# Performance work log

Hardware: AMD Instinct MI355X
Metric: run time of the kernel (lower is better)

The kernel has to match this reference:

```python
import jax, jax.numpy as jnp
import numpy as np

EPS = 1e-5
KH = KW = 3
PAD = 1

def conv3x3(x, w, b=None):
    out = jax.lax.conv_general_dilated(
        x, w, window_strides=(1, 1), padding=((PAD, PAD), (PAD, PAD)),
        dimension_numbers=("NCHW", "OIHW", "NCHW"))
    if b is not None:
        out = out + b[None, :, None, None]
    return out

def batchnorm(x, gamma, beta):
    # training-mode BatchNorm2d: batch statistics over (N, H, W)
    mean = x.mean(axis=(0, 2, 3), keepdims=True)
    var = x.var(axis=(0, 2, 3), keepdims=True)
    return gamma[None, :, None, None] * (x - mean) / jnp.sqrt(var + EPS) + beta[None, :, None, None]

def bilinear_gather(x, y_pos, x_pos):
    # x: [B,C,H,W]; y_pos/x_pos: [B,P,H,W] (P = KH*KW sampling taps)
    # zero padding outside image (mmcv modulated deform conv semantics)
    B, C, H, W = x.shape
    P = y_pos.shape[1]
    x_flat = x.reshape(B, C, H * W)
    y0 = jnp.floor(y_pos)
    x0 = jnp.floor(x_pos)
    ly = y_pos - y0
    lx = x_pos - x0
    out = jnp.zeros((B, C, P, H, W), dtype=x.dtype)
    for dy, dx, wgt in ((0, 0, (1 - ly) * (1 - lx)), (0, 1, (1 - ly) * lx),
                        (1, 0, ly * (1 - lx)), (1, 1, ly * lx)):
        yi = y0 + dy
        xi = x0 + dx
        valid = ((yi >= 0) & (yi <= H - 1) & (xi >= 0) & (xi <= W - 1)).astype(x.dtype)
        yc = jnp.clip(yi, 0, H - 1).astype(jnp.int32)
        xc = jnp.clip(xi, 0, W - 1).astype(jnp.int32)
        idx = (yc * W + xc).reshape(B, 1, P * H * W)
        vals = jnp.take_along_axis(x_flat, jnp.broadcast_to(idx, (B, C, P * H * W)), axis=2)
        vals = vals.reshape(B, C, P, H, W)
        out = out + vals * (wgt * valid)[:, None]
    return out  # [B,C,P,H,W]

def modulated_deform_conv(x, w_off, b_off, w_dcn):
    B, C, H, W = x.shape
    P = KH * KW
    off = conv3x3(x, w_off, b_off)  # [B, 3*P, H, W]
    o1, o2, m = jnp.split(off, 3, axis=1)
    offset = jnp.concatenate([o1, o2], axis=1)            # [B, 2P, H, W]
    offset = offset.reshape(B, P, 2, H, W)                # channel 2p -> dy, 2p+1 -> dx
    mask = jax.nn.sigmoid(m)                              # [B, P, H, W]
    hh = jnp.arange(H, dtype=x.dtype)
    ww = jnp.arange(W, dtype=x.dtype)
    ky = jnp.arange(KH, dtype=x.dtype)
    kx = jnp.arange(KW, dtype=x.dtype)
    # base sampling grid per tap p = ky*KW + kx: (h - PAD + ky, w - PAD + kx)
    base_y = (hh[None, :] - PAD + ky[:, None])            # [KH, H]
    base_x = (ww[None, :] - PAD + kx[:, None])            # [KW, W]
    base_y = jnp.broadcast_to(base_y[:, None, :, None], (KH, KW, H, W)).reshape(P, H, W)
    base_x = jnp.broadcast_to(base_x[None, :, None, :], (KH, KW, H, W)).reshape(P, H, W)
    y_pos = base_y[None] + offset[:, :, 0]                # [B,P,H,W]
    x_pos = base_x[None] + offset[:, :, 1]
    sampled = bilinear_gather(x, y_pos, x_pos)            # [B,C,P,H,W]
    sampled = sampled * mask[:, None]
    w = w_dcn.reshape(w_dcn.shape[0], C, P)               # [O, C, P]
    return jnp.einsum("bcphw,ocp->bohw", sampled, w)

def setup_inputs() -> dict:
    key = jax.random.key(0)
    ks = jax.random.split(key, 10)
    B, Ch, H, W = 4, 256, 64, 64
    Cin, Cout = 2 * Ch, 256
    P = KH * KW
    inp = {
        "input_v": jax.random.normal(ks[0], (B, Ch, H, W), jnp.float32),
        "input_i": jax.random.normal(ks[1], (B, Ch, H, W), jnp.float32),
        "w_off": jax.random.normal(ks[2], (3 * P, Cin, KH, KW), jnp.float32) * 0.01,
        "b_off": jnp.zeros((3 * P,), jnp.float32),
        "w_dcn": jax.random.normal(ks[3], (Cout, Cin, KH, KW), jnp.float32) * (1.0 / np.sqrt(Cin * P)),
        "gamma1": jnp.ones((Cout,), jnp.float32),
        "beta1": jnp.zeros((Cout,), jnp.float32),
        "w2": jax.random.normal(ks[4], (Cout, Cout, KH, KW), jnp.float32) * (1.0 / np.sqrt(Cout * P)),
        "gamma2": jnp.ones((Cout,), jnp.float32),
        "beta2": jnp.zeros((Cout,), jnp.float32),
    }
    return inp

def reference(input_v, input_i, w_off, b_off, w_dcn, gamma1, beta1, w2, gamma2, beta2):
    x = jnp.concatenate([input_v, input_i], axis=1)
    out = modulated_deform_conv(x, w_off, b_off, w_dcn)
    out = jax.nn.relu(batchnorm(out, gamma1, beta1))
    out = jax.nn.relu(batchnorm(conv3x3(out, w2), gamma2, beta2))
    return out
```

## Files before the change

### kernel.cpp

```cpp
#include <hip/hip_runtime.h>
#include <cstdint>
#include <cstddef>

typedef unsigned short u16;
typedef __attribute__((ext_vector_type(8))) short s16x8;
typedef __attribute__((ext_vector_type(4))) float f32x4;

#define DEV __device__ __forceinline__

DEV float bf2f(short u){
  union { unsigned int i; float f; } v;
  v.i = ((unsigned int)(u16)u) << 16;
  return v.f;
}
DEV short f2bf(float f){
  union { float f; unsigned int i; } v; v.f = f;
  unsigned int u = v.i;
  u += 0x7fffu + ((u >> 16) & 1u);
  return (short)(u >> 16);
}
DEV f32x4 f32x4_zero(){
  f32x4 z;
#pragma unroll
  for(int j=0;j<4;j++) z[j]=0.f;
  return z;
}
DEV f32x4 mfma16(s16x8 a, s16x8 b, f32x4 c){
  return __builtin_amdgcn_mfma_f32_16x16x32_bf16(a, b, c, 0, 0, 0);
}
DEV void cp16(const void* g, void* l){
  __builtin_amdgcn_global_load_lds(
      (const __attribute__((address_space(1))) unsigned int*)g,
      (__attribute__((address_space(3))) unsigned int*)l, 16, 0, 0);
}

static constexpr size_t OFF_ACC_B   = 0;
static constexpr size_t OUT1_ACC_B  = 2097152;
static constexpr size_t OUT2_ACC_B  = 18874368;
static constexpr size_t STATS_B     = 35651584;
static constexpr size_t ZERO_BYTES  = 35655680;
static constexpr size_t XN_PAD_B    = 35655680;
static constexpr size_t OUT1N_PAD_B = 53497856;
static constexpr size_t WOFFT_B     = 62418944;
static constexpr size_t WDCNT_B     = 62713856;
static constexpr size_t W2T_B       = 65073152;
static constexpr size_t SAMP_O_B    = 66252800;
static constexpr size_t SAMP_W_B    = 68612096;
static constexpr size_t A_SAMP_B    = 70971392;

__global__ void k_border(u16* __restrict__ xp, u16* __restrict__ op){
  const int cid = blockIdx.x, t = threadIdx.x;
  const int b = cid / 260, rem = cid % 260;
  int y, x;
  if(rem < 132){ y = (rem/66)*65; x = rem%66; }
  else { int r2 = rem-132; x = (r2>>6)*65; y = 1 + (r2&63); }
  const size_t cell = (size_t)(b*66+y)*66 + x;
  ((unsigned int*)(xp + cell*512))[t] = 0;
  if(t < 128) ((unsigned int*)(op + cell*256))[t] = 0;
}

__global__ void k_x_to_nhwc(const float* __restrict__ v, const float* __restrict__ vi,
                            u16* __restrict__ xn){
  __shared__ float tile[64][65];
  const int b = blockIdx.z, c0 = blockIdx.y*64, h = blockIdx.x;
  const float* src = (c0 < 256) ? (v  + ((size_t)b*256 + c0)      *4096)
                                : (vi + ((size_t)b*256 + (c0-256))*4096);
  const int t = threadIdx.x;
#pragma unroll
  for(int k=0;k<16;k++){
    int idx = t + k*256;
    int cl = idx >> 6, wl = idx & 63;
    tile[cl][wl] = src[(size_t)cl*4096 + h*64 + wl];
  }
  __syncthreads();
#pragma unroll
  for(int k=0;k<16;k++){
    int idx = t + k*256;
    int wl = idx >> 6, cl = idx & 63;
    xn[((size_t)(b*66 + h+1)*66 + (wl+1))*512 + c0 + cl] = (u16)f2bf(tile[cl][wl]);
  }
}

__global__ void k_prep_woff(const float* __restrict__ w, u16* __restrict__ wt){
  int i = blockIdx.x*256 + threadIdx.x;
  if(i >= 147456) return;
  int j = i & 7, n = (i>>3) & 31, kcp = i>>8;
  int kc = kcp & 63, tp = kcp >> 6;
  int c = kc*8 + j;
  float val = (n < 27) ? w[(size_t)(n*512 + c)*9 + tp] : 0.f;
  wt[i] = (u16)f2bf(val);
}
__global__ void k_prep_wdcn(const float* __restrict__ w, u16* __restrict__ wt){
  int i = blockIdx.x*256 + threadIdx.x;
  if(i >= 1179648) return;
  int j = i & 7, n = (i>>3) & 255, kcp = i>>11;
  int kc = kcp & 63, tp = kcp >> 6;
  int c = kc*8 + j;
  wt[i] = (u16)f2bf(w[(size_t)(n*512 + c)*9 + tp]);
}
__global__ void k_prep_w2(const float* __restrict__ w, u16* __restrict__ wt){
  int i = blockIdx.x*256 + threadIdx.x;
  if(i >= 589824) return;
  int j = i & 7, n = (i>>3) & 255, kcp = i>>11;
  int kc = kcp & 31, tp = kcp >> 5;
  int c = kc*8 + j;
  wt[i] = (u16)f2bf(w[(size_t)(n*256 + c)*9 + tp]);
}

__global__ __launch_bounds__(256, 6) void k_conv_off(
    const u16* __restrict__ xn, const u16* __restrict__ wt, float* __restrict__ offa){
  __shared__ short A[2][4][64][8];
  __shared__ short B[2][4][32][8];
  const int tid = threadIdx.x;
  const int lane = tid & 63, wid = tid >> 6;
  const int quad = lane >> 4, ln = lane & 15;
  const int m0 = blockIdx.x * 64;
  const int b = m0 >> 12, h = (m0 >> 6) & 63;
  const int gst0 = blockIdx.y * 24;
  const int m_base = wid * 16;
  f32x4 acc0 = f32x4_zero(), acc1 = f32x4_zero();

  {
    const int tp = gst0 >> 4, s = gst0 & 15;
    const int ty = tp/3, tx = tp - ty*3;
    cp16(xn + ((size_t)(b*66 + h+ty)*66 + lane + tx)*512 + s*32 + wid*8, &A[0][wid][0][0]);
    if(wid < 2)
      cp16(wt + ((size_t)tp*64 + s*4)*256 + wid*512 + lane*8, (short*)&B[0][0][0][0] + wid*512);
  }
  __syncthreads();

  int buf = 0;
  for(int it=0; it<24; it++){
    const int nb = buf ^ 1;
    if(it < 23){
      const int gn = gst0 + it + 1;
      const int tp = gn >> 4, s = gn & 15;
      const int ty = tp/3, tx = tp - ty*3;
      cp16(xn + ((size_t)(b*66 + h+ty)*66 + lane + tx)*512 + s*32 + wid*8, &A[nb][wid][0][0]);
      if(wid < 2)
        cp16(wt + ((size_t)tp*64 + s*4)*256 + wid*512 + lane*8, (short*)&B[nb][0][0][0] + wid*512);
    }
    const s16x8* Ap = (const s16x8*)&A[buf][0][0][0];
    const s16x8* Bp = (const s16x8*)&B[buf][0][0][0];
    s16x8 a  = Ap[quad*64 + m_base + ln];
    s16x8 b0 = Bp[quad*32 + ln];
    s16x8 b1 = Bp[quad*32 + 16 + ln];
    acc0 = mfma16(a, b0, acc0);
    acc1 = mfma16(a, b1, acc1);
    __syncthreads();
    buf = nb;
  }
#pragma unroll
  for(int nf=0;nf<2;nf++){
    const f32x4 v = nf ? acc1 : acc0;
    const int col = nf*16 + ln;
#pragma unroll
    for(int i=0;i<4;i++){
      const int row = m_base + quad*4 + i;
      unsafeAtomicAdd(offa + (size_t)(m0+row)*32 + col, v[i]);
    }
  }
}

__global__ void k_sampler(const float* __restrict__ offa, const float* __restrict__ boff,
                          int* __restrict__ so, float* __restrict__ sw){
  const int idx = blockIdx.x*256 + threadIdx.x;
  if(idx >= 16384*9) return;
  const int m = idx / 9, tp = idx - m*9;
  const int b = m >> 12, h = (m >> 6) & 63, w = m & 63;
  const float* orow = offa + (size_t)m*32;
  float dy = orow[2*tp]   + boff[2*tp];
  float dx = orow[2*tp+1] + boff[2*tp+1];
  float mz = orow[18+tp]  + boff[18+tp];
  float mk = 1.f / (1.f + expf(-mz));
  float ypos = (float)(h - 1 + tp/3) + dy;
  float xpos = (float)(w - 1 + tp%3) + dx;
  float y0f = floorf(ypos), x0f = floorf(xpos);
  float ly = ypos - y0f, lx = xpos - x0f;
  int y0 = (int)y0f, x0 = (int)x0f;
#pragma unroll
  for(int k=0;k<4;k++){
    int ddy = k >> 1, ddx = k & 1;
    int yi = y0 + ddy, xi = x0 + ddx;
    bool vv = (yi >= 0) & (yi < 64) & (xi >= 0) & (xi < 64);
    float wk = (ddy ? ly : 1.f-ly) * (ddx ? lx : 1.f-lx) * mk;
    if(!vv) wk = 0.f;
    int yc = yi < 0 ? 0 : (yi > 63 ? 63 : yi);
    int xc = xi < 0 ? 0 : (xi > 63 ? 63 : xi);
    so[(size_t)idx*4 + k] = ((b*66 + yc+1)*66 + xc+1) << 9;
    sw[(size_t)idx*4 + k] = wk;
  }
}

__global__ __launch_bounds__(256) void k_sample_a(
    const u16* __restrict__ xn, const int* __restrict__ so, const float* __restrict__ sw,
    u16* __restrict__ as){
  const int blk = blockIdx.x;
  const int pb = ((blk & 7) << 5) | (blk >> 3);
  const int m = pb*64 + (threadIdx.x >> 2);
  const int q = threadIdx.x & 3;
  for(int tp=0; tp<9; tp++){
    const int4   po = *(const int4*)  (so + ((size_t)m*9 + tp)*4);
    const float4 pw = *(const float4*)(sw + ((size_t)m*9 + tp)*4);
    const u16* x0 = xn + po.x + q*8;
    const u16* x1 = xn + po.y + q*8;
    const u16* x2 = xn + po.z + q*8;
    const u16* x3 = xn + po.w + q*8;
    u16* dst = as + (size_t)m*4608 + tp*512 + q*8;
#pragma unroll 4
    for(int u=0; u<16; u++){
      const int c0 = u*32;
      s16x8 g0 = *(const s16x8*)(x0 + c0);
      s16x8 g1 = *(const s16x8*)(x1 + c0);
      s16x8 g2 = *(const s16x8*)(x2 + c0);
      s16x8 g3 = *(const s16x8*)(x3 + c0);
      s16x8 pk;
#pragma unroll
      for(int j=0;j<8;j++){
        float f = pw.x * bf2f(g0[j]);
        f = fmaf(pw.y, bf2f(g1[j]), f);
        f = fmaf(pw.z, bf2f(g2[j]), f);
        f = fmaf(pw.w, bf2f(g3[j]), f);
        pk[j] = f2bf(f);
      }
      *(s16x8*)(dst + c0) = pk;
    }
  }
}

__global__ __launch_bounds__(256, 4) void k_dcn_gemm(
    const u16* __restrict__ as, const u16* __restrict__ wt, float* __restrict__ outa){
  __shared__ short A[2][4][64][8];
  __shared__ short B[2][4][256][8];
  const int tid = threadIdx.x;
  const int lane = tid & 63, wid = tid >> 6;
  const int quad = lane >> 4, ln = lane & 15;
  const int m0 = blockIdx.x * 64;
  const int gst0 = blockIdx.y * 48;
  const int m_base = (wid >> 1)*32, n_base = (wid & 1)*128;
  f32x4 acc[2][8];
#pragma unroll
  for(int mf=0;mf<2;mf++)
#pragma unroll
    for(int nf=0;nf<8;nf++) acc[mf][nf] = f32x4_zero();

  const u16* arow = as + (size_t)(m0 + lane)*4608;

  {
    const int tp = gst0 >> 4, s = gst0 & 15;
    cp16(arow + gst0*32 + wid*8, &A[0][wid][0][0]);
    const u16* bs = wt + ((size_t)tp*64 + s*4)*2048 + (wid*4)*512 + lane*8;
    short* bd = (short*)&B[0][0][0][0] + (wid*4)*512;
#pragma unroll
    for(int i=0;i<4;i++) cp16(bs + i*512, bd + i*512);
  }
  __syncthreads();

  int buf = 0;
  for(int it=0; it<48; it++){
    const int nb = buf ^ 1;
    if(it < 47){
      const int gn = gst0 + it + 1;
      const int tp = gn >> 4, s = gn & 15;
      cp16(arow + gn*32 + wid*8, &A[nb][wid][0][0]);
      const u16* bs = wt + ((size_t)tp*64 + s*4)*2048 + (wid*4)*512 + lane*8;
      short* bd = (short*)&B[nb][0][0][0] + (wid*4)*512;
#pragma unroll
      for(int i=0;i<4;i++) cp16(bs + i*512, bd + i*512);
    }
    const s16x8* Ap = (const s16x8*)&A[buf][0][0][0];
    const s16x8* Bp = (const s16x8*)&B[buf][0][0][0];
    s16x8 a0 = Ap[quad*64 + m_base + ln];
    s16x8 a1 = Ap[quad*64 + m_base + 16 + ln];
#pragma unroll
    for(int nf=0;nf<8;nf++){
      s16x8 bf = Bp[quad*256 + n_base + nf*16 + ln];
      acc[0][nf] = mfma16(a0, bf, acc[0][nf]);
      acc[1][nf] = mfma16(a1, bf, acc[1][nf]);
    }
    __syncthreads();
    buf = nb;
  }
#pragma unroll
  for(int mf=0;mf<2;mf++)
#pragma unroll
    for(int nf=0;nf<8;nf++){
      const int col = n_base + nf*16 + ln;
#pragma unroll
      for(int i=0;i<4;i++){
        const int row = m_base + mf*16 + quad*4 + i;
        unsafeAtomicAdd(outa + (size_t)(m0+row)*256 + col, acc[mf][nf][i]);
      }
    }
}

__global__ __launch_bounds__(256, 4) void k_conv2(
    const u16* __restrict__ a_in, const u16* __restrict__ wt, float* __restrict__ outa){
  __shared__ short A[2][4][64][8];
  __shared__ short B[2][4][256][8];
  const int tid = threadIdx.x;
  const int lane = tid & 63, wid = tid >> 6;
  const int quad = lane >> 4, ln = lane & 15;
  const int m0 = blockIdx.x * 64;
  const int b = m0 >> 12, h = (m0 >> 6) & 63;
  const int gst0 = blockIdx.y * 24;
  const int m_base = (wid >> 1)*32, n_base = (wid & 1)*128;
  f32x4 acc[2][8];
#pragma unroll
  for(int mf=0;mf<2;mf++)
#pragma unroll
    for(int nf=0;nf<8;nf++) acc[mf][nf] = f32x4_zero();

  {
    const int tp = gst0 >> 3, s = gst0 & 7;
    const int ty = tp/3, tx = tp - ty*3;
    cp16(a_in + ((size_t)(b*66 + h+ty)*66 + lane + tx)*256 + s*32 + wid*8, &A[0][wid][0][0]);
    const u16* bs = wt + ((size_t)tp*32 + s*4)*2048 + (wid*4)*512 + lane*8;
    short* bd = (short*)&B[0][0][0][0] + (wid*4)*512;
#pragma unroll
    for(int i=0;i<4;i++) cp16(bs + i*512, bd + i*512);
  }
  __syncthreads();

  int buf = 0;
  for(int it=0; it<24; it++){
    const int nb = buf ^ 1;
    if(it < 23){
      const int gn = gst0 + it + 1;
      const int tp = gn >> 3, s = gn & 7;
      const int ty = tp/3, tx = tp - ty*3;
      cp16(a_in + ((size_t)(b*66 + h+ty)*66 + lane + tx)*256 + s*32 + wid*8, &A[nb][wid][0][0]);
      const u16* bs = wt + ((size_t)tp*32 + s*4)*2048 + (wid*4)*512 + lane*8;
      short* bd = (short*)&B[nb][0][0][0] + (wid*4)*512;
#pragma unroll
      for(int i=0;i<4;i++) cp16(bs + i*512, bd + i*512);
    }
    const s16x8* Ap = (const s16x8*)&A[buf][0][0][0];
    const s16x8* Bp = (const s16x8*)&B[buf][0][0][0];
    s16x8 a0 = Ap[quad*64 + m_base + ln];
    s16x8 a1 = Ap[quad*64 + m_base + 16 + ln];
#pragma unroll
    for(int nf=0;nf<8;nf++){
      s16x8 bf = Bp[quad*256 + n_base + nf*16 + ln];
      acc[0][nf] = mfma16(a0, bf, acc[0][nf]);
      acc[1][nf] = mfma16(a1, bf, acc[1][nf]);
    }
    __syncthreads();
    buf = nb;
  }
#pragma unroll
  for(int mf=0;mf<2;mf++)
#pragma unroll
    for(int nf=0;nf<8;nf++){
      const int col = n_base + nf*16 + ln;
#pragma unroll
      for(int i=0;i<4;i++){
        const int row = m_base + mf*16 + quad*4 + i;
        unsafeAtomicAdd(outa + (size_t)(m0+row)*256 + col, acc[mf][nf][i]);
      }
    }
}

__global__ void k_stats(const float* __restrict__ acc, float* __restrict__ sum,
                        float* __restrict__ sq){
  const int m0 = blockIdx.x*64;
  const int c = threadIdx.x;
  float s = 0.f, q = 0.f;
  for(int i=0;i<64;i++){
    float v = acc[(size_t)(m0+i)*256 + c];
    s += v; q += v*v;
  }
  unsafeAtomicAdd(sum + c, s);
  unsafeAtomicAdd(sq + c, q);
}

__global__ void k_bn1(const float* __restrict__ acc, const float* __restrict__ sum,
                      const float* __restrict__ sq, const float* __restrict__ g,
                      const float* __restrict__ bt, u16* __restrict__ o){
  __shared__ float sc[256], sh[256];
  const int t = threadIdx.x;
  {
    float mean = sum[t] * (1.f/16384.f);
    float var  = sq[t] * (1.f/16384.f) - mean*mean;
    float rstd = rsqrtf(var + 1e-5f);
    float s = g[t] * rstd;
    sc[t] = s; sh[t] = bt[t] - mean*s;
  }
  __syncthreads();
  const int c4 = (t & 63) * 4;
  const float s0 = sc[c4], s1 = sc[c4+1], s2 = sc[c4+2], s3 = sc[c4+3];
  const float h0 = sh[c4], h1 = sh[c4+1], h2 = sh[c4+2], h3 = sh[c4+3];
#pragma unroll
  for(int k=0;k<4;k++){
    int m = blockIdx.x*16 + k*4 + (t>>6);
    int b = m >> 12, hh = (m >> 6) & 63, ww = m & 63;
    const float4 v = *(const float4*)(acc + (size_t)m*256 + c4);
    unsigned int lo = (unsigned int)(u16)f2bf(fmaxf(0.f, v.x*s0 + h0))
                    | ((unsigned int)(u16)f2bf(fmaxf(0.f, v.y*s1 + h1)) << 16);
    unsigned int hi = (unsigned int)(u16)f2bf(fmaxf(0.f, v.z*s2 + h2))
                    | ((unsigned int)(u16)f2bf(fmaxf(0.f, v.w*s3 + h3)) << 16);
    uint2 pr; pr.x = lo; pr.y = hi;
    *(uint2*)(o + ((size_t)(b*66 + hh+1)*66 + ww+1)*256 + c4) = pr;
  }
}

__global__ void k_bn2_out(const float* __restrict__ acc, const float* __restrict__ sum,
                          const float* __restrict__ sq, const float* __restrict__ g,
                          const float* __restrict__ bt, float* __restrict__ out){
  __shared__ float tile[64][65];
  __shared__ float sc[64], sh[64];
  const int t = threadIdx.x;
  const int b = blockIdx.z, c0 = blockIdx.y*64, hw0 = blockIdx.x*64;
  if(t < 64){
    int c = c0 + t;
    float mean = sum[c] * (1.f/16384.f);
    float var  = sq[c] * (1.f/16384.f) - mean*mean;
    float rstd = rsqrtf(var + 1e-5f);
    float s = g[c] * rstd;
    sc[t] = s; sh[t] = bt[c] - mean*s;
  }
  __syncthreads();
#pragma unroll
  for(int k=0;k<16;k++){
    int idx = t + k*256;
    int wl = idx >> 6, cl = idx & 63;
    float v = acc[(size_t)((b<<12) + hw0 + wl)*256 + c0 + cl];
    tile[wl][cl] = fmaxf(0.f, v*sc[cl] + sh[cl]);
  }
  __syncthreads();
#pragma unroll
  for(int k=0;k<16;k++){
    int idx = t + k*256;
    int cl = idx >> 6, wl = idx & 63;
    out[(size_t)(b*256 + c0 + cl)*4096 + hw0 + wl] = tile[wl][cl];
  }
}

extern "C" void kernel_launch(void* const* d_in, const int* in_sizes, int n_in,
                              void* d_out, int out_size, void* d_ws, size_t ws_size,
                              hipStream_t stream){
  const float* in_v  = (const float*)d_in[0];
  const float* in_i  = (const float*)d_in[1];
  const float* w_off = (const float*)d_in[2];
  const float* b_off = (const float*)d_in[3];
  const float* w_dcn = (const float*)d_in[4];
  const float* g1    = (const float*)d_in[5];
  const float* bt1   = (const float*)d_in[6];
  const float* w2    = (const float*)d_in[7];
  const float* g2    = (const float*)d_in[8];
  const float* bt2   = (const float*)d_in[9];
  float* out = (float*)d_out;
  char* ws = (char*)d_ws;

  float* off_acc  = (float*)(ws + OFF_ACC_B);
  float* out1_acc = (float*)(ws + OUT1_ACC_B);
  float* out2_acc = (float*)(ws + OUT2_ACC_B);
  float* stats    = (float*)(ws + STATS_B);
  float* sum1 = stats,       *sq1 = stats + 256;
  float* sum2 = stats + 512, *sq2 = stats + 768;
  u16* xn_pad    = (u16*)(ws + XN_PAD_B);
  u16* out1n_pad = (u16*)(ws + OUT1N_PAD_B);
  u16* wofft = (u16*)(ws + WOFFT_B);
  u16* wdcnt = (u16*)(ws + WDCNT_B);
  u16* w2t   = (u16*)(ws + W2T_B);
  int*   samp_o = (int*)(ws + SAMP_O_B);
  float* samp_w = (float*)(ws + SAMP_W_B);
  u16* a_samp = (u16*)(ws + A_SAMP_B);

  hipMemsetAsync(ws, 0, ZERO_BYTES, stream);
  k_border<<<1040, 256, 0, stream>>>(xn_pad, out1n_pad);
  k_x_to_nhwc<<<dim3(64,8,4), 256, 0, stream>>>(in_v, in_i, xn_pad);
  k_prep_woff<<<576, 256, 0, stream>>>(w_off, wofft);
  k_prep_wdcn<<<4608, 256, 0, stream>>>(w_dcn, wdcnt);
  k_prep_w2<<<2304, 256, 0, stream>>>(w2, w2t);
  k_conv_off<<<dim3(256,6), 256, 0, stream>>>(xn_pad, wofft, off_acc);
  k_sampler<<<576, 256, 0, stream>>>(off_acc, b_off, samp_o, samp_w);
  k_sample_a<<<256, 256, 0, stream>>>(xn_pad, samp_o, samp_w, a_samp);
  k_dcn_gemm<<<dim3(256,3), 256, 0, stream>>>(a_samp, wdcnt, out1_acc);
  k_stats<<<256, 256, 0, stream>>>(out1_acc, sum1, sq1);
  k_bn1<<<1024, 256, 0, stream>>>(out1_acc, sum1, sq1, g1, bt1, out1n_pad);
  k_conv2<<<dim3(256,3), 256, 0, stream>>>(out1n_pad, w2t, out2_acc);
  k_stats<<<256, 256, 0, stream>>>(out2_acc, sum2, sq2);
  k_bn2_out<<<dim3(64,4,4), 256, 0, stream>>>(out2_acc, sum2, sq2, g2, bt2, out);
}
```

Measured before the change: 393.1 us.

## Retile DCN and conv2 GEMMs to 128x128 and split sampling per tap

Both implicit-GEMM kernels move from a 64x256 output tile with a 32-wide K step and double-buffered LDS to a 128x128 tile with a 64-wide K step. Each wave now computes a 4x4 grid of MFMA fragments, and the grid gains a split-K z dimension. LDS staging becomes single-buffered with two barriers per iteration, so loads no longer overlap compute. The launch bound drops to 3 blocks per CU. Separately, the sampling kernel assigns one tap per block instead of looping over all 9, giving 9x more blocks to raise parallelism for the gather.

Result: faster. 382.0 us (-2.8%).

```diff
diff --git a/kernel.cpp b/kernel.cpp
--- a/kernel.cpp
+++ b/kernel.cpp
@@ -196,167 +196,166 @@
     const u16* __restrict__ xn, const int* __restrict__ so, const float* __restrict__ sw,
     u16* __restrict__ as){
   const int blk = blockIdx.x;
-  const int pb = ((blk & 7) << 5) | (blk >> 3);
+  const int x = blk & 7, g = blk >> 3;
+  const int tp = g >> 5, pbi = g & 31;
+  const int pb = x*32 + pbi;
   const int m = pb*64 + (threadIdx.x >> 2);
   const int q = threadIdx.x & 3;
-  for(int tp=0; tp<9; tp++){
-    const int4   po = *(const int4*)  (so + ((size_t)m*9 + tp)*4);
-    const float4 pw = *(const float4*)(sw + ((size_t)m*9 + tp)*4);
-    const u16* x0 = xn + po.x + q*8;
-    const u16* x1 = xn + po.y + q*8;
-    const u16* x2 = xn + po.z + q*8;
-    const u16* x3 = xn + po.w + q*8;
-    u16* dst = as + (size_t)m*4608 + tp*512 + q*8;
+  const int4   po = *(const int4*)  (so + ((size_t)m*9 + tp)*4);
+  const float4 pw = *(const float4*)(sw + ((size_t)m*9 + tp)*4);
+  const u16* x0 = xn + po.x + q*8;
+  const u16* x1 = xn + po.y + q*8;
+  const u16* x2 = xn + po.z + q*8;
+  const u16* x3 = xn + po.w + q*8;
+  u16* dst = as + (size_t)m*4608 + tp*512 + q*8;
 #pragma unroll 4
-    for(int u=0; u<16; u++){
-      const int c0 = u*32;
-      s16x8 g0 = *(const s16x8*)(x0 + c0);
-      s16x8 g1 = *(const s16x8*)(x1 + c0);
-      s16x8 g2 = *(const s16x8*)(x2 + c0);
-      s16x8 g3 = *(const s16x8*)(x3 + c0);
-      s16x8 pk;
-#pragma unroll
-      for(int j=0;j<8;j++){
-        float f = pw.x * bf2f(g0[j]);
-        f = fmaf(pw.y, bf2f(g1[j]), f);
-        f = fmaf(pw.z, bf2f(g2[j]), f);
-        f = fmaf(pw.w, bf2f(g3[j]), f);
-        pk[j] = f2bf(f);
-      }
-      *(s16x8*)(dst + c0) = pk;
-    }
-  }
-}
-
-__global__ __launch_bounds__(256, 4) void k_dcn_gemm(
+  for(int u=0; u<16; u++){
+    const int c0 = u*32;
+    s16x8 g0 = *(const s16x8*)(x0 + c0);
+    s16x8 g1 = *(const s16x8*)(x1 + c0);
+    s16x8 g2 = *(const s16x8*)(x2 + c0);
+    s16x8 g3 = *(const s16x8*)(x3 + c0);
+    s16x8 pk;
+#pragma unroll
+    for(int j=0;j<8;j++){
+      float f = pw.x * bf2f(g0[j]);
+      f = fmaf(pw.y, bf2f(g1[j]), f);
+      f = fmaf(pw.z, bf2f(g2[j]), f);
+      f = fmaf(pw.w, bf2f(g3[j]), f);
+      pk[j] = f2bf(f);
+    }
+    *(s16x8*)(dst + c0) = pk;
+  }
+}
+
+__global__ __launch_bounds__(256, 3) void k_dcn_gemm(
     const u16* __restrict__ as, const u16* __restrict__ wt, float* __restrict__ outa){
-  __shared__ short A[2][4][64][8];
-  __shared__ short B[2][4][256][8];
+  __shared__ short A[8][128][8];
+  __shared__ short B[8][128][8];
   const int tid = threadIdx.x;
   const int lane = tid & 63, wid = tid >> 6;
   const int quad = lane >> 4, ln = lane & 15;
-  const int m0 = blockIdx.x * 64;
-  const int gst0 = blockIdx.y * 48;
-  const int m_base = (wid >> 1)*32, n_base = (wid & 1)*128;
-  f32x4 acc[2][8];
-#pragma unroll
-  for(int mf=0;mf<2;mf++)
-#pragma unroll
-    for(int nf=0;nf<8;nf++) acc[mf][nf] = f32x4_zero();
-
-  const u16* arow = as + (size_t)(m0 + lane)*4608;
-
-  {
-    const int tp = gst0 >> 4, s = gst0 & 15;
-    cp16(arow + gst0*32 + wid*8, &A[0][wid][0][0]);
-    const u16* bs = wt + ((size_t)tp*64 + s*4)*2048 + (wid*4)*512 + lane*8;
-    short* bd = (short*)&B[0][0][0][0] + (wid*4)*512;
-#pragma unroll
-    for(int i=0;i<4;i++) cp16(bs + i*512, bd + i*512);
-  }
-  __syncthreads();
-
-  int buf = 0;
-  for(int it=0; it<48; it++){
-    const int nb = buf ^ 1;
-    if(it < 47){
-      const int gn = gst0 + it + 1;
-      const int tp = gn >> 4, s = gn & 15;
-      cp16(arow + gn*32 + wid*8, &A[nb][wid][0][0]);
-      const u16* bs = wt + ((size_t)tp*64 + s*4)*2048 + (wid*4)*512 + lane*8;
-      short* bd = (short*)&B[nb][0][0][0] + (wid*4)*512;
-#pragma unroll
-      for(int i=0;i<4;i++) cp16(bs + i*512, bd + i*512);
-    }
-    const s16x8* Ap = (const s16x8*)&A[buf][0][0][0];
-    const s16x8* Bp = (const s16x8*)&B[buf][0][0][0];
-    s16x8 a0 = Ap[quad*64 + m_base + ln];
-    s16x8 a1 = Ap[quad*64 + m_base + 16 + ln];
-#pragma unroll
-    for(int nf=0;nf<8;nf++){
-      s16x8 bf = Bp[quad*256 + n_base + nf*16 + ln];
-      acc[0][nf] = mfma16(a0, bf, acc[0][nf]);
-      acc[1][nf] = mfma16(a1, bf, acc[1][nf]);
+  const int m0 = blockIdx.x * 128, n0 = blockIdx.y * 128;
+  const int it0 = blockIdx.z * 24;
+  const int m_w = (wid >> 1)*64, n_w = (wid & 1)*64;
+  const s16x8* Ap = (const s16x8*)A;
+  const s16x8* Bp = (const s16x8*)B;
+  f32x4 acc[4][4];
+#pragma unroll
+  for(int mf=0;mf<4;mf++)
+#pragma unroll
+    for(int nf=0;nf<4;nf++) acc[mf][nf] = f32x4_zero();
+
+  const u16* arow0 = as + (size_t)(m0 + lane)*4608;
+  const u16* arow1 = as + (size_t)(m0 + 64 + lane)*4608;
+
+  for(int it=0; it<24; it++){
+    const int k0 = (it0 + it)*64;
+#pragma unroll
+    for(int i=0;i<4;i++){
+      const int tt = wid*4 + i, kc = tt >> 1, rh = tt & 1;
+      cp16((rh ? arow1 : arow0) + k0 + kc*8, &A[kc][rh*64][0]);
+    }
+#pragma unroll
+    for(int i=0;i<4;i++){
+      const int tt = wid*4 + i, kc = tt >> 1, nh = tt & 1;
+      cp16(wt + ((size_t)((k0>>3) + kc)*256 + n0 + nh*64 + lane)*8, &B[kc][nh*64][0]);
     }
     __syncthreads();
-    buf = nb;
-  }
-#pragma unroll
-  for(int mf=0;mf<2;mf++)
-#pragma unroll
-    for(int nf=0;nf<8;nf++){
-      const int col = n_base + nf*16 + ln;
+#pragma unroll
+    for(int ks=0; ks<2; ks++){
+      s16x8 af[4], bf[4];
+#pragma unroll
+      for(int mf=0;mf<4;mf++) af[mf] = Ap[(ks*4+quad)*128 + m_w + mf*16 + ln];
+#pragma unroll
+      for(int nf=0;nf<4;nf++) bf[nf] = Bp[(ks*4+quad)*128 + n_w + nf*16 + ln];
+#pragma unroll
+      for(int mf=0;mf<4;mf++)
+#pragma unroll
+        for(int nf=0;nf<4;nf++)
+          acc[mf][nf] = mfma16(af[mf], bf[nf], acc[mf][nf]);
+    }
+    __syncthreads();
+  }
+#pragma unroll
+  for(int mf=0;mf<4;mf++)
+#pragma unroll
+    for(int nf=0;nf<4;nf++){
+      const int col = n0 + n_w + nf*16 + ln;
 #pragma unroll
       for(int i=0;i<4;i++){
-        const int row = m_base + mf*16 + quad*4 + i;
-        unsafeAtomicAdd(outa + (size_t)(m0+row)*256 + col, acc[mf][nf][i]);
+        const int row = m0 + m_w + mf*16 + quad*4 + i;
+        unsafeAtomicAdd(outa + (size_t)row*256 + col, acc[mf][nf][i]);
       }
     }
 }
 
-__global__ __launch_bounds__(256, 4) void k_conv2(
+__global__ __launch_bounds__(256, 3) void k_conv2(
     const u16* __restrict__ a_in, const u16* __restrict__ wt, float* __restrict__ outa){
-  __shared__ short A[2][4][64][8];
-  __shared__ short B[2][4][256][8];
+  __shared__ short A[8][128][8];
+  __shared__ short B[8][128][8];
   const int tid = threadIdx.x;
   const int lane = tid & 63, wid = tid >> 6;
   const int quad = lane >> 4, ln = lane & 15;
-  const int m0 = blockIdx.x * 64;
-  const int b = m0 >> 12, h = (m0 >> 6) & 63;
-  const int gst0 = blockIdx.y * 24;
-  const int m_base = (wid >> 1)*32, n_base = (wid & 1)*128;
-  f32x4 acc[2][8];
-#pragma unroll
-  for(int mf=0;mf<2;mf++)
-#pragma unroll
-    for(int nf=0;nf<8;nf++) acc[mf][nf] = f32x4_zero();
-
-  {
-    const int tp = gst0 >> 3, s = gst0 & 7;
+  const int m0 = blockIdx.x * 128, n0 = blockIdx.y * 128;
+  const int it0 = blockIdx.z * 12;
+  const int m_w = (wid >> 1)*64, n_w = (wid & 1)*64;
+  const s16x8* Ap = (const s16x8*)A;
+  const s16x8* Bp = (const s16x8*)B;
+  f32x4 acc[4][4];
+#pragma unroll
+  for(int mf=0;mf<4;mf++)
+#pragma unroll
+    for(int nf=0;nf<4;nf++) acc[mf][nf] = f32x4_zero();
+
+  int cell[2];
+#pragma unroll
+  for(int rh=0; rh<2; rh++){
+    const int m = m0 + rh*64 + lane;
+    const int b = m >> 12, h = (m >> 6) & 63, w = m & 63;
+    cell[rh] = (b*66 + h)*66 + w;
+  }
+
+  for(int it=0; it<12; it++){
+    const int k0 = (it0 + it)*64;
+    const int tp = k0 >> 8;
     const int ty = tp/3, tx = tp - ty*3;
-    cp16(a_in + ((size_t)(b*66 + h+ty)*66 + lane + tx)*256 + s*32 + wid*8, &A[0][wid][0][0]);
-    const u16* bs = wt + ((size_t)tp*32 + s*4)*2048 + (wid*4)*512 + lane*8;
-    short* bd = (short*)&B[0][0][0][0] + (wid*4)*512;
-#pragma unroll
-    for(int i=0;i<4;i++) cp16(bs + i*512, bd + i*512);
-  }
-  __syncthreads();
-
-  int buf = 0;
-  for(int it=0; it<24; it++){
-    const int nb = buf ^ 1;
-    if(it < 23){
-      const int gn = gst0 + it + 1;
-      const int tp = gn >> 3, s = gn & 7;
-      const int ty = tp/3, tx = tp - ty*3;
-      cp16(a_in + ((size_t)(b*66 + h+ty)*66 + lane + tx)*256 + s*32 + wid*8, &A[nb][wid][0][0]);
-      const u16* bs = wt + ((size_t)tp*32 + s*4)*2048 + (wid*4)*512 + lane*8;
-      short* bd = (short*)&B[nb][0][0][0] + (wid*4)*512;
-#pragma unroll
-      for(int i=0;i<4;i++) cp16(bs + i*512, bd + i*512);
-    }
-    const s16x8* Ap = (const s16x8*)&A[buf][0][0][0];
-    const s16x8* Bp = (const s16x8*)&B[buf][0][0][0];
-    s16x8 a0 = Ap[quad*64 + m_base + ln];
-    s16x8 a1 = Ap[quad*64 + m_base + 16 + ln];
-#pragma unroll
-    for(int nf=0;nf<8;nf++){
-      s16x8 bf = Bp[quad*256 + n_base + nf*16 + ln];
-      acc[0][nf] = mfma16(a0, bf, acc[0][nf]);
-      acc[1][nf] = mfma16(a1, bf, acc[1][nf]);
+    const int kb8 = (k0 & 255) >> 3;
+#pragma unroll
+    for(int i=0;i<4;i++){
+      const int tt = wid*4 + i, kc = tt >> 1, rh = tt & 1;
+      cp16(a_in + ((size_t)(cell[rh] + ty*66 + tx))*256 + (kb8 + kc)*8, &A[kc][rh*64][0]);
+    }
+#pragma unroll
+    for(int i=0;i<4;i++){
+      const int tt = wid*4 + i, kc = tt >> 1, nh = tt & 1;
+      cp16(wt + ((size_t)((k0>>3) + kc)*256 + n0 + nh*64 + lane)*8, &B[kc][nh*64][0]);
     }
     __syncthreads();
-    buf = nb;
-  }
-#pragma unroll
-  for(int mf=0;mf<2;mf++)
-#pragma unroll
-    for(int nf=0;nf<8;nf++){
-      const int col = n_base + nf*16 + ln;
+#pragma unroll
+    for(int ks=0; ks<2; ks++){
+      s16x8 af[4], bf[4];
+#pragma unroll
+      for(int mf=0;mf<4;mf++) af[mf] = Ap[(ks*4+quad)*128 + m_w + mf*16 + ln];
+#pragma unroll
+      for(int nf=0;nf<4;nf++) bf[nf] = Bp[(ks*4+quad)*128 + n_w + nf*16 + ln];
+#pragma unroll
+      for(int mf=0;mf<4;mf++)
+#pragma unroll
+        for(int nf=0;nf<4;nf++)
+          acc[mf][nf] = mfma16(af[mf], bf[nf], acc[mf][nf]);
+    }
+    __syncthreads();
+  }
+#pragma unroll
+  for(int mf=0;mf<4;mf++)
+#pragma unroll
+    for(int nf=0;nf<4;nf++){
+      const int col = n0 + n_w + nf*16 + ln;
 #pragma unroll
       for(int i=0;i<4;i++){
-        const int row = m_base + mf*16 + quad*4 + i;
-        unsafeAtomicAdd(outa + (size_t)(m0+row)*256 + col, acc[mf][nf][i]);
+        const int row = m0 + m_w + mf*16 + quad*4 + i;
+        unsafeAtomicAdd(outa + (size_t)row*256 + col, acc[mf][nf][i]);
       }
     }
 }
@@ -475,11 +474,11 @@
   k_prep_w2<<<2304, 256, 0, stream>>>(w2, w2t);
   k_conv_off<<<dim3(256,6), 256, 0, stream>>>(xn_pad, wofft, off_acc);
   k_sampler<<<576, 256, 0, stream>>>(off_acc, b_off, samp_o, samp_w);
-  k_sample_a<<<256, 256, 0, stream>>>(xn_pad, samp_o, samp_w, a_samp);
-  k_dcn_gemm<<<dim3(256,3), 256, 0, stream>>>(a_samp, wdcnt, out1_acc);
+  k_sample_a<<<2304, 256, 0, stream>>>(xn_pad, samp_o, samp_w, a_samp);
+  k_dcn_gemm<<<dim3(128,2,3), 256, 0, stream>>>(a_samp, wdcnt, out1_acc);
   k_stats<<<256, 256, 0, stream>>>(out1_acc, sum1, sq1);
   k_bn1<<<1024, 256, 0, stream>>>(out1_acc, sum1, sq1, g1, bt1, out1n_pad);
-  k_conv2<<<dim3(256,3), 256, 0, stream>>>(out1n_pad, w2t, out2_acc);
+  k_conv2<<<dim3(128,2,3), 256, 0, stream>>>(out1n_pad, w2t, out2_acc);
   k_stats<<<256, 256, 0, stream>>>(out2_acc, sum2, sq2);
   k_bn2_out<<<dim3(64,4,4), 256, 0, stream>>>(out2_acc, sum2, sq2, g2, bt2, out);
 }
```
